# Kernel tuning notes

Hardware: AMD Instinct MI355X
Metric: run time of the kernel (lower is better)

## Reference

```python
import jax, jax.numpy as jnp
import numpy as np

D = 4  # max_displacement

def setup_inputs() -> dict:
    key = jax.random.key(0)
    k1, k2 = jax.random.split(key)
    fa = jax.random.normal(k1, (8, 256, 96, 128), dtype=jnp.float32)
    fb = jax.random.normal(k2, (8, 256, 96, 128), dtype=jnp.float32)
    return {"fa": fa, "fb": fb}

def _l2_normalize(x):
    # matches torch F.normalize(p=2, dim=1, eps=1e-12)
    n = jnp.sqrt(jnp.sum(x * x, axis=1, keepdims=True))
    return x / jnp.maximum(n, 1e-12)

def reference(fa, fb):
    B, C, H, W = fa.shape
    d = D
    fa = _l2_normalize(fa)
    fb = _l2_normalize(fb)
    fbp = jnp.pad(fb, ((0, 0), (0, 0), (d, d), (d, d)))
    # fixed small loop over (2d+1)^2 = 81 shifts; each dot is (B,H,W)
    corr = [
        jnp.sum(fa * jax.lax.dynamic_slice(fbp, (0, 0, dy, dx), (B, C, H, W)), axis=1)
        for dy in range(2 * d + 1)
        for dx in range(2 * d + 1)
    ]
    return jnp.stack(corr, axis=1)  # (B, (2d+1)^2, H, W)
```

## Files before the change

kernel.cpp:

```cpp
#include <hip/hip_runtime.h>
#include <math.h>

namespace {
constexpr int Bn = 8, Cn = 256, Hn = 96, Wn = 128;
constexpr int HWn = Hn * Wn;
constexpr int CHWn = Cn * HWn;
constexpr int Kn = 81;
constexpr int TW = 32, TH = 6;
constexpr int HR = TH + 8;
constexpr int HC = TW + 8;
constexpr int HCP = 44;
constexpr int CC = 8;
constexpr int NTHREADS = 8 * 9 * 6;
constexpr int HALO = HR * HC;
}

__global__ __launch_bounds__(NTHREADS, 4)
void corr81_kernel(const float* __restrict__ fa,
                   const float* __restrict__ fb,
                   float* __restrict__ out) {
  __shared__ __align__(16) float lfb[CC][HR][HCP];
  __shared__ float ssb[HALO];

  const int tx = threadIdx.x;
  const int g  = threadIdx.y;
  const int ty = threadIdx.z;
  const int tid = tx + 8 * g + 72 * ty;

  const int flat = blockIdx.x;
  const int o = (flat & 7) * 64 + (flat >> 3);
  const int b  = o >> 6;
  const int r  = o & 63;
  const int h0 = (r >> 2) * TH;
  const int w0 = (r & 3) * TW;
  const int wb = w0 + 4 * tx;

  for (int i = tid; i < HALO; i += NTHREADS) ssb[i] = 0.0f;

  float acc[9][4];
  #pragma unroll
  for (int k = 0; k < 9; ++k) {
    #pragma unroll
    for (int j = 0; j < 4; ++j) acc[k][j] = 0.0f;
  }
  float ssa[4] = {0.f, 0.f, 0.f, 0.f};

  const float* faP = fa + (size_t)b * CHWn + (h0 + ty) * Wn + wb;

  int   s_hr[2], s_hc[2];
  bool  s_on[2], s_ok[2];
  const float* s_ptr[2];
  #pragma unroll
  for (int i = 0; i < 2; ++i) {
    int px = tid + NTHREADS * i;
    s_on[i] = (px < HALO);
    int hr = px / HC, hc = px - hr * HC;
    s_hr[i] = hr; s_hc[i] = hc;
    int gh = h0 - 4 + hr, gw = w0 - 4 + hc;
    s_ok[i] = s_on[i] && gh >= 0 && gh < Hn && gw >= 0 && gw < Wn;
    s_ptr[i] = fb + (size_t)b * CHWn + (size_t)gh * Wn + gw;
  }
  __syncthreads();

  for (int c0 = 0; c0 < Cn; c0 += CC) {
    #pragma unroll
    for (int i = 0; i < 2; ++i) {
      if (s_on[i]) {
        float ss = 0.f;
        if (s_ok[i]) {
          const float* p = s_ptr[i] + (size_t)c0 * HWn;
          #pragma unroll
          for (int cc = 0; cc < CC; ++cc) {
            float v = p[(size_t)cc * HWn];
            lfb[cc][s_hr[i]][s_hc[i]] = v;
            ss += v * v;
          }
        } else {
          #pragma unroll
          for (int cc = 0; cc < CC; ++cc) lfb[cc][s_hr[i]][s_hc[i]] = 0.f;
        }
        ssb[s_hr[i] * HC + s_hc[i]] += ss;
      }
    }
    float4 areg[CC];
    #pragma unroll
    for (int cc = 0; cc < CC; ++cc)
      areg[cc] = *(const float4*)(faP + (size_t)(c0 + cc) * HWn);
    __syncthreads();

    #pragma unroll
    for (int cc = 0; cc < CC; ++cc) {
      const float a0 = areg[cc].x, a1 = areg[cc].y, a2 = areg[cc].z, a3 = areg[cc].w;
      ssa[0] += a0 * a0; ssa[1] += a1 * a1; ssa[2] += a2 * a2; ssa[3] += a3 * a3;
      const float* rowp = &lfb[cc][ty + g][4 * tx];
      const float4 wa = *(const float4*)(rowp);
      const float4 wv = *(const float4*)(rowp + 4);
      const float4 wc = *(const float4*)(rowp + 8);
      const float win[12] = {wa.x, wa.y, wa.z, wa.w,
                             wv.x, wv.y, wv.z, wv.w,
                             wc.x, wc.y, wc.z, wc.w};
      #pragma unroll
      for (int dx = 0; dx < 9; ++dx) {
        acc[dx][0] += a0 * win[dx + 0];
        acc[dx][1] += a1 * win[dx + 1];
        acc[dx][2] += a2 * win[dx + 2];
        acc[dx][3] += a3 * win[dx + 3];
      }
    }
    __syncthreads();
  }

  for (int i = tid; i < HALO; i += NTHREADS) {
    ssb[i] = 1.0f / fmaxf(sqrtf(ssb[i]), 1e-12f);
  }
  float rna[4];
  #pragma unroll
  for (int j = 0; j < 4; ++j) rna[j] = 1.0f / fmaxf(sqrtf(ssa[j]), 1e-12f);
  __syncthreads();

  float* outP = out + (size_t)b * (Kn * HWn) + (h0 + ty) * Wn + wb;
  const int rr = ty + g;
  #pragma unroll
  for (int dx = 0; dx < 9; ++dx) {
    const int k = g * 9 + dx;
    float4 v;
    v.x = acc[dx][0] * rna[0] * ssb[rr * HC + 4 * tx + dx + 0];
    v.y = acc[dx][1] * rna[1] * ssb[rr * HC + 4 * tx + dx + 1];
    v.z = acc[dx][2] * rna[2] * ssb[rr * HC + 4 * tx + dx + 2];
    v.w = acc[dx][3] * rna[3] * ssb[rr * HC + 4 * tx + dx + 3];
    *(float4*)(outP + (size_t)k * HWn) = v;
  }
}

extern "C" void kernel_launch(void* const* d_in, const int* in_sizes, int n_in,
                              void* d_out, int out_size, void* d_ws, size_t ws_size,
                              hipStream_t stream) {
  const float* fa = (const float*)d_in[0];
  const float* fb = (const float*)d_in[1];
  float* outp = (float*)d_out;
  dim3 grid(512);
  dim3 block(8, 9, 6);
  hipLaunchKernelGGL(corr81_kernel, grid, block, 0, stream, fa, fb, outp);
}
```

Baseline: 275.7 us.

## Split channel reduction across two thread groups per block with shared-memory combine

Doubles the block to two sub-groups that each accumulate correlations and norms over half of the channels, using separate shared tiles. Partial accumulators are then combined through shared memory in two staged passes, and only the first group writes the output. This is meant to raise wave count per CU and latency hiding for the 512-block grid. In exchange it adds a reduction phase with extra barriers, larger shared memory per block, and register pressure from the tighter launch bound.

After: 604.6 us. 2.19x slower.

```diff
diff --git a/kernel.cpp b/kernel.cpp
--- a/kernel.cpp
+++ b/kernel.cpp
@@ -11,21 +11,28 @@
 constexpr int HC = TW + 8;
 constexpr int HCP = 44;
 constexpr int CC = 8;
-constexpr int NTHREADS = 8 * 9 * 6;
+constexpr int KS = 2;
+constexpr int CHALF = Cn / KS;
+constexpr int NSUB = 8 * 9 * 6;
+constexpr int NTHREADS = NSUB * KS;
 constexpr int HALO = HR * HC;
+constexpr int SCRS = 21;
 }
 
-__global__ __launch_bounds__(NTHREADS, 4)
+__global__ __launch_bounds__(NTHREADS, 7)
 void corr81_kernel(const float* __restrict__ fa,
                    const float* __restrict__ fb,
                    float* __restrict__ out) {
-  __shared__ __align__(16) float lfb[CC][HR][HCP];
-  __shared__ float ssb[HALO];
+  __shared__ __align__(16) float lfb[KS][CC][HR][HCP];
+  __shared__ float ssb[KS][HALO];
 
   const int tx = threadIdx.x;
   const int g  = threadIdx.y;
-  const int ty = threadIdx.z;
-  const int tid = tx + 8 * g + 72 * ty;
+  const int tz = threadIdx.z;
+  const int ty = tz % 6;
+  const int ks = tz / 6;
+  const int stid = tx + 8 * g + 72 * ty;
+  const int tid  = tx + 8 * (g + 9 * tz);
 
   const int flat = blockIdx.x;
   const int o = (flat & 7) * 64 + (flat >> 3);
@@ -35,7 +42,7 @@
   const int w0 = (r & 3) * TW;
   const int wb = w0 + 4 * tx;
 
-  for (int i = tid; i < HALO; i += NTHREADS) ssb[i] = 0.0f;
+  for (int i = tid; i < KS * HALO; i += NTHREADS) (&ssb[0][0])[i] = 0.0f;
 
   float acc[9][4];
   #pragma unroll
@@ -45,24 +52,26 @@
   }
   float ssa[4] = {0.f, 0.f, 0.f, 0.f};
 
-  const float* faP = fa + (size_t)b * CHWn + (h0 + ty) * Wn + wb;
+  const float* faP = fa + (size_t)b * CHWn + (size_t)(ks * CHALF) * HWn
+                   + (h0 + ty) * Wn + wb;
 
   int   s_hr[2], s_hc[2];
   bool  s_on[2], s_ok[2];
   const float* s_ptr[2];
   #pragma unroll
   for (int i = 0; i < 2; ++i) {
-    int px = tid + NTHREADS * i;
+    int px = stid + NSUB * i;
     s_on[i] = (px < HALO);
     int hr = px / HC, hc = px - hr * HC;
     s_hr[i] = hr; s_hc[i] = hc;
     int gh = h0 - 4 + hr, gw = w0 - 4 + hc;
     s_ok[i] = s_on[i] && gh >= 0 && gh < Hn && gw >= 0 && gw < Wn;
-    s_ptr[i] = fb + (size_t)b * CHWn + (size_t)gh * Wn + gw;
+    s_ptr[i] = fb + (size_t)b * CHWn + (size_t)(ks * CHALF) * HWn
+             + (size_t)gh * Wn + gw;
   }
   __syncthreads();
 
-  for (int c0 = 0; c0 < Cn; c0 += CC) {
+  for (int c0 = 0; c0 < CHALF; c0 += CC) {
     #pragma unroll
     for (int i = 0; i < 2; ++i) {
       if (s_on[i]) {
@@ -72,14 +81,14 @@
           #pragma unroll
           for (int cc = 0; cc < CC; ++cc) {
             float v = p[(size_t)cc * HWn];
-            lfb[cc][s_hr[i]][s_hc[i]] = v;
+            lfb[ks][cc][s_hr[i]][s_hc[i]] = v;
             ss += v * v;
           }
         } else {
           #pragma unroll
-          for (int cc = 0; cc < CC; ++cc) lfb[cc][s_hr[i]][s_hc[i]] = 0.f;
+          for (int cc = 0; cc < CC; ++cc) lfb[ks][cc][s_hr[i]][s_hc[i]] = 0.f;
         }
-        ssb[s_hr[i] * HC + s_hc[i]] += ss;
+        ssb[ks][s_hr[i] * HC + s_hc[i]] += ss;
       }
     }
     float4 areg[CC];
@@ -92,7 +101,7 @@
     for (int cc = 0; cc < CC; ++cc) {
       const float a0 = areg[cc].x, a1 = areg[cc].y, a2 = areg[cc].z, a3 = areg[cc].w;
       ssa[0] += a0 * a0; ssa[1] += a1 * a1; ssa[2] += a2 * a2; ssa[3] += a3 * a3;
-      const float* rowp = &lfb[cc][ty + g][4 * tx];
+      const float* rowp = &lfb[ks][cc][ty + g][4 * tx];
       const float4 wa = *(const float4*)(rowp);
       const float4 wv = *(const float4*)(rowp + 4);
       const float4 wc = *(const float4*)(rowp + 8);
@@ -110,25 +119,59 @@
     __syncthreads();
   }
 
-  for (int i = tid; i < HALO; i += NTHREADS) {
-    ssb[i] = 1.0f / fmaxf(sqrtf(ssb[i]), 1e-12f);
-  }
-  float rna[4];
-  #pragma unroll
-  for (int j = 0; j < 4; ++j) rna[j] = 1.0f / fmaxf(sqrtf(ssa[j]), 1e-12f);
+  for (int i = tid; i < HALO; i += NTHREADS)
+    ssb[0][i] = 1.0f / fmaxf(sqrtf(ssb[0][i] + ssb[1][i]), 1e-12f);
   __syncthreads();
 
-  float* outP = out + (size_t)b * (Kn * HWn) + (h0 + ty) * Wn + wb;
-  const int rr = ty + g;
-  #pragma unroll
-  for (int dx = 0; dx < 9; ++dx) {
-    const int k = g * 9 + dx;
-    float4 v;
-    v.x = acc[dx][0] * rna[0] * ssb[rr * HC + 4 * tx + dx + 0];
-    v.y = acc[dx][1] * rna[1] * ssb[rr * HC + 4 * tx + dx + 1];
-    v.z = acc[dx][2] * rna[2] * ssb[rr * HC + 4 * tx + dx + 2];
-    v.w = acc[dx][3] * rna[3] * ssb[rr * HC + 4 * tx + dx + 3];
-    *(float4*)(outP + (size_t)k * HWn) = v;
+  float* scr = &lfb[0][0][0][0];
+  if (ks == 1) {
+    #pragma unroll
+    for (int dx = 0; dx < 4; ++dx)
+      #pragma unroll
+      for (int j = 0; j < 4; ++j) scr[stid * SCRS + dx * 4 + j] = acc[dx][j];
+    #pragma unroll
+    for (int j = 0; j < 4; ++j) scr[stid * SCRS + 16 + j] = ssa[j];
+  }
+  __syncthreads();
+  if (ks == 0) {
+    #pragma unroll
+    for (int dx = 0; dx < 4; ++dx)
+      #pragma unroll
+      for (int j = 0; j < 4; ++j) acc[dx][j] += scr[stid * SCRS + dx * 4 + j];
+    #pragma unroll
+    for (int j = 0; j < 4; ++j) ssa[j] += scr[stid * SCRS + 16 + j];
+  }
+  __syncthreads();
+  if (ks == 1) {
+    #pragma unroll
+    for (int dx = 4; dx < 9; ++dx)
+      #pragma unroll
+      for (int j = 0; j < 4; ++j) scr[stid * SCRS + (dx - 4) * 4 + j] = acc[dx][j];
+  }
+  __syncthreads();
+
+  if (ks == 0) {
+    #pragma unroll
+    for (int dx = 4; dx < 9; ++dx)
+      #pragma unroll
+      for (int j = 0; j < 4; ++j) acc[dx][j] += scr[stid * SCRS + (dx - 4) * 4 + j];
+
+    float rna[4];
+    #pragma unroll
+    for (int j = 0; j < 4; ++j) rna[j] = 1.0f / fmaxf(sqrtf(ssa[j]), 1e-12f);
+
+    float* outP = out + (size_t)b * (Kn * HWn) + (h0 + ty) * Wn + wb;
+    const int rr = ty + g;
+    #pragma unroll
+    for (int dx = 0; dx < 9; ++dx) {
+      const int k = g * 9 + dx;
+      float4 v;
+      v.x = acc[dx][0] * rna[0] * ssb[0][rr * HC + 4 * tx + dx + 0];
+      v.y = acc[dx][1] * rna[1] * ssb[0][rr * HC + 4 * tx + dx + 1];
+      v.z = acc[dx][2] * rna[2] * ssb[0][rr * HC + 4 * tx + dx + 2];
+      v.w = acc[dx][3] * rna[3] * ssb[0][rr * HC + 4 * tx + dx + 3];
+      *(float4*)(outP + (size_t)k * HWn) = v;
+    }
   }
 }
 
@@ -139,6 +182,6 @@
   const float* fb = (const float*)d_in[1];
   float* outp = (float*)d_out;
   dim3 grid(512);
-  dim3 block(8, 9, 6);
+  dim3 block(8, 9, 12);
   hipLaunchKernelGGL(corr81_kernel, grid, block, 0, stream, fa, fb, outp);
 }
```
